# Optimization experiments

Measured on AMD Instinct MI355X. Metric: run time of the kernel, lower is better.

## Reference

```python
import jax, jax.numpy as jnp
import numpy as np
from jax import lax

K = 32768          # queue size
C = 100            # num_classes == len(cls_num_list1)
B = 1024           # batch size (features.shape[0] - K)
D = 128            # embedding dim
ALPHA = 0.05; BETA = 1.0; GAMMA = 1.0; SUPT = 1.0
T = 0.07; BASE_T = 0.07   # base_temperature defaults to temperature
SMOOTH = 0.0; EPS = 1e-12


def setup_inputs() -> dict:
    key = jax.random.key(0)
    k1, k2, k3, k4 = jax.random.split(key, 4)
    features = jax.random.normal(k1, (B + K, D), dtype=jnp.float32)
    features = features / jnp.linalg.norm(features, axis=1, keepdims=True)  # contrastive feats are L2-normalized
    centers = jax.random.normal(k2, (C, D), dtype=jnp.float32)
    centers = centers / jnp.linalg.norm(centers, axis=1, keepdims=True)
    sup_logits = jax.random.normal(k3, (B, C), dtype=jnp.float32)
    labels = jax.random.randint(k4, (B + K,), 0, C, dtype=jnp.int32)
    return {"features": features, "sup_logits": sup_logits, "centers": centers, "labels": labels}


def _loss(features, sup_logits, centers, labels):
    f32 = features.dtype
    lab_c = jnp.arange(C, dtype=labels.dtype)
    lab1 = jnp.concatenate([labels[:B], lab_c])                 # [B+C]
    mask = (labels[:B, None] == labels[None, :]).astype(f32)    # [B, B+K]
    mask1 = (lab1[:B, None] == lab1[None, :]).astype(f32)       # [B, B+C]
    # class counts over batch+queue (batch_cls_count) and batch+centers (batch_cls_count1)
    cls_count = jnp.zeros((C,), f32).at[labels].add(1.0)
    cls_count1 = jnp.zeros((C,), f32).at[lab1].add(1.0)
    diag = jnp.arange(B)
    logits_mask = jnp.ones((B, B + K), f32).at[diag, diag].set(0.0)
    logits_mask1 = jnp.ones((B, B + C), f32).at[diag, diag].set(0.0)
    mask = mask * logits_mask
    mask1 = mask1 * logits_mask1

    # ---- branch 1: batch anchors vs [batch, class centers] ----
    feats1 = jnp.concatenate([features[:B], centers], axis=0)   # [B+C, D]
    logits1 = (features[:B] @ feats1.T) / T                     # [B, B+C]
    logits1 = logits1 - lax.stop_gradient(logits1.max(axis=1, keepdims=True))
    exp1 = jnp.exp(logits1) * logits_mask1
    w1 = cls_count1[lab1][None, :] - mask1                      # per-instance class weight
    denom1 = (exp1 / w1).sum(axis=1, keepdims=True)
    log_prob1 = logits1 - jnp.log(denom1 + EPS)
    loss1 = -jnp.mean((mask1 * log_prob1).sum(1) / mask1.sum(1))

    # ---- branch 2: [sup_logits, batch anchors vs batch+queue] ----
    adc = (features[:B] @ features.T) / T                       # [B, B+K]
    logits = jnp.concatenate([sup_logits / SUPT, adc], axis=1)  # [B, C+B+K] (self.weight is None)
    logits = logits - lax.stop_gradient(logits.max(axis=1, keepdims=True))
    one_hot = jax.nn.one_hot(labels[:B], C, dtype=f32)
    one_hot = SMOOTH / (C - 1) * (1.0 - one_hot) + (1.0 - SMOOTH) * one_hot
    mask_full = jnp.concatenate([one_hot * BETA, mask * ALPHA], axis=1)
    lmask_full = jnp.concatenate([jnp.ones((B, C), f32), GAMMA * logits_mask], axis=1)
    expl = jnp.exp(logits) * lmask_full
    lab_full = jnp.concatenate([lab_c, labels])                 # [C+B+K]
    w = cls_count[lab_full][None, :] - mask_full
    denom = (expl / w).sum(axis=1, keepdims=True)
    log_prob = logits - jnp.log(denom + EPS)
    loss2 = -(T / BASE_T) * jnp.mean((mask_full * log_prob).sum(1) / mask_full.sum(1))
    return loss1 + loss2


def reference(features, sup_logits, centers, labels):
    return _loss(features, sup_logits, centers, labels)
```

## Files before the change

kernel.cpp:

```cpp
#include <hip/hip_runtime.h>
#include <math.h>

#define KQ   32768
#define CC   100
#define BB   1024
#define DD   128
#define NTOT (BB + KQ)
#define CB_CENT 1056
#define NCB  1060
#define NHIST 33
#define NCG2 132
#define CG_SUP 141
#define NSL  141

#define INV_T  14.285714285714286f
#define K2E    20.609929f
#define ALPHA  0.05f
#define EPSV   1e-12f

typedef __attribute__((ext_vector_type(8)))  short          short8;
typedef __attribute__((ext_vector_type(8)))  unsigned short ushort8;
typedef __attribute__((ext_vector_type(16))) float          float16;

__device__ __forceinline__ unsigned short f2bf_rne(float f) {
    unsigned int u = __float_as_uint(f);
    return (unsigned short)((u + 0x7FFFu + ((u >> 16) & 1u)) >> 16);
}


__global__ __launch_bounds__(256) void prep_k(const float* __restrict__ feats,
                                              const float* __restrict__ centers,
                                              const int* __restrict__ labels,
                                              unsigned short* __restrict__ X2,
                                              int* __restrict__ cntP,
                                              int* __restrict__ cntB) {
    const int b = blockIdx.x, t = threadIdx.x;
    if (b >= NCB) {
        const int h = b - NCB;
        __shared__ int hA[CC], hB[CC];
        if (t < CC) { hA[t] = 0; hB[t] = 0; }
        __syncthreads();
        const int base = h * 1024;
#pragma unroll
        for (int q = 0; q < 4; ++q) {
            int l = labels[base + q * 256 + t];
            atomicAdd(&hA[l], 1);
            if (h == 0) atomicAdd(&hB[l], 1);
        }
        __syncthreads();
        if (t < 128) {
            cntP[h * 128 + t] = (t < CC) ? hA[t] : 0;
            if (h == 0) cntB[t] = (t < CC) ? hB[t] : 0;
        }
        return;
    }
    __shared__ unsigned short sm[8 * 66 * 8];
    const int rl = t >> 3, c8 = t & 7;
    const int r = b * 32 + rl;
    const float* src;
    if (r < NTOT)            src = &feats[(size_t)r * DD];
    else if (r < NTOT + CC)  src = &centers[(size_t)(r - NTOT) * DD];
    else                     src = nullptr;
#pragma unroll
    for (int s = 0; s < 2; ++s) {
        const int c8p = c8 + 8 * s;
        float v[8];
        if (src) {
            const float4* p = (const float4*)(src + c8p * 8);
            float4 q0 = p[0], q1 = p[1];
            v[0]=q0.x; v[1]=q0.y; v[2]=q0.z; v[3]=q0.w;
            v[4]=q1.x; v[5]=q1.y; v[6]=q1.z; v[7]=q1.w;
        } else {
#pragma unroll
            for (int j = 0; j < 8; ++j) v[j] = 0.f;
        }
        ushort8 H;
#pragma unroll
        for (int m = 0; m < 8; ++m) H[m] = f2bf_rne(v[m]);
        const int ks = c8p >> 1, lh = c8p & 1;
        *(ushort8*)&sm[(ks * 66 + rl + 32 * lh) * 8] = H;
    }
    __syncthreads();
    ushort8* dst = (ushort8*)((char*)X2 + (size_t)b * 8192);
#pragma unroll
    for (int j = 0; j < 2; ++j) {
        const int idx = j * 256 + t;
        const int ks = idx >> 6, ln = idx & 63;
        dst[idx] = *(const ushort8*)&sm[(ks * 66 + ln) * 8];
    }
}

__device__ __forceinline__ void epi_tile(
    const float16& acc, int cb, int lc, float rn, float drm, bool checkDiag,
    int half, int ln, int growbase, const int* rlab, float* sS, float* sN)
{
    const int ccol = cb * 32 + ln;
#pragma unroll
    for (int reg = 0; reg < 16; ++reg) {
        int ro = (reg & 3) + 8 * (reg >> 2) + 4 * half;
        float a  = acc[reg];
        float mf = (lc == rlab[reg]) ? 1.f : 0.f;
        float wgt = fmaf(mf, drm, rn);
        if (checkDiag) {
            bool d = (ccol == growbase + ro);
            wgt = d ? 0.f : wgt;
            mf  = d ? 0.f : mf;
        }
        float e = exp2f(fmaf(a, K2E, -K2E));
        sS[reg] = fmaf(e, wgt, sS[reg]);
        sN[reg] = fmaf(mf, a, sN[reg]);
    }
}

__device__ __forceinline__ void pair_tiles(
    const char* Xb, int cb0, int cb1,
    int lc0, float rn0, float drm0, bool dg0,
    int lc1, float rn1, float drm1, bool dg1,
    int lane, int half, int ln, int growbase,
    const short8* Ah, const int* rlab, float* sS, float* sN)
{
    const size_t b0 = (size_t)cb0 * 8192 + (size_t)lane * 16;
    const size_t b1 = (size_t)cb1 * 8192 + (size_t)lane * 16;
    float16 a0, a1;
#pragma unroll
    for (int reg = 0; reg < 16; ++reg) { a0[reg] = 0.f; a1[reg] = 0.f; }
#pragma unroll
    for (int ks = 0; ks < 8; ++ks) {
        short8 B0 = *(const short8*)(Xb + b0 + (size_t)ks * 1024);
        short8 B1 = *(const short8*)(Xb + b1 + (size_t)ks * 1024);
        a0 = __builtin_amdgcn_mfma_f32_32x32x16_bf16(Ah[ks], B0, a0, 0, 0, 0);
        a1 = __builtin_amdgcn_mfma_f32_32x32x16_bf16(Ah[ks], B1, a1, 0, 0, 0);
    }
    epi_tile(a0, cb0, lc0, rn0, drm0, dg0, half, ln, growbase, rlab, sS, sN);
    epi_tile(a1, cb1, lc1, rn1, drm1, dg1, half, ln, growbase, rlab, sS, sN);
}

__global__ __launch_bounds__(256) void gemm_k(
    const unsigned short* __restrict__ X2, const int* __restrict__ labels,
    const int* __restrict__ cntP, const int* __restrict__ cntB,
    const float* __restrict__ sup,
    float* __restrict__ pS, float* __restrict__ pN,
    float* __restrict__ supS, float* __restrict__ supLi) {
    const int b = blockIdx.x;
    const int xcd = b & 7, l = b >> 3;
    const int rt = l & 7, ci = l >> 3;
    const int cg = xcd + 8 * ci;
    if (cg > CG_SUP) return;

    const int tid = threadIdx.x;
    const int lane = tid & 63, w = tid >> 6;
    const int half = lane >> 5, ln = lane & 31;
    const char* Xb = (const char*)X2;

    __shared__ float cntAF[128], rnA[128], drmA[128], rn1S[128], drm1S[128];
    if (tid < 128) {
        int s = 0;
#pragma unroll
        for (int h = 0; h < NHIST; ++h) s += cntP[h * 128 + tid];
        float cf = (float)s;
        cntAF[tid] = cf;
        float rn = __builtin_amdgcn_rcpf(fmaxf(cf, 1.f));
        rnA[tid] = (s > 0) ? __builtin_amdgcn_rcpf(cf) : 0.f;
        drmA[tid] = (s > 0) ? (__builtin_amdgcn_rcpf(cf - ALPHA) - rnA[tid]) : 0.f;
        (void)rn;
        int sb = cntB[tid];
        float c1 = (float)(sb + 1);
        float rn1 = __builtin_amdgcn_rcpf(c1);
        rn1S[tid] = rn1;
        drm1S[tid] = __builtin_amdgcn_rcpf(fmaxf(c1 - 1.f, 1.f)) - rn1;
    }
    __syncthreads();

    if (cg == CG_SUP) {
        const int g = rt * 4 + w;
        const int c0 = lane, c1 = lane + 64;
        float n0 = cntAF[c0];
        float rA0 = __builtin_amdgcn_rcpf(n0);
        float rAm0 = __builtin_amdgcn_rcpf(fmaxf(n0 - 1.f, 1.f));
        float rA1 = 0.f, rAm1 = 0.f;
        if (lane < 36) {
            float n1 = cntAF[c1];
            rA1 = __builtin_amdgcn_rcpf(n1);
            rAm1 = __builtin_amdgcn_rcpf(fmaxf(n1 - 1.f, 1.f));
        }
        for (int rr = 0; rr < 32; ++rr) {
            int row = g * 32 + rr;
            int li = labels[row];
            const float* srow = &sup[(size_t)row * CC];
            float v0 = srow[c0];
            float s = __expf(v0 - INV_T) * ((c0 == li) ? rAm0 : rA0);
            float liv = (c0 == li) ? v0 : 0.f;
            if (lane < 36) {
                float v1 = srow[c1];
                s += __expf(v1 - INV_T) * ((c1 == li) ? rAm1 : rA1);
                liv += (c1 == li) ? v1 : 0.f;
            }
#pragma unroll
            for (int off = 1; off < 64; off <<= 1) {
                s += __shfl_xor(s, off, 64);
                liv += __shfl_xor(liv, off, 64);
            }
            if (lane == 0) { supS[row] = s; supLi[row] = liv; }
        }
        return;
    }

    const int rb = rt * 4 + w;
    const int growbase = rt * 128 + w * 32;
    short8 Ah[8];
    {
        size_t abase = (size_t)rb * 8192 + (size_t)lane * 16;
#pragma unroll
        for (int ks = 0; ks < 8; ++ks)
            Ah[ks] = *(const short8*)(Xb + abase + (size_t)ks * 1024);
    }
    int rlab[16];
#pragma unroll
    for (int reg = 0; reg < 16; ++reg) {
        int ro = (reg & 3) + 8 * (reg >> 2) + 4 * half;
        rlab[reg] = labels[growbase + ro];
    }
    float sS[16], sN[16];
#pragma unroll
    for (int reg = 0; reg < 16; ++reg) { sS[reg] = 0.f; sN[reg] = 0.f; }

    const bool isB2 = (cg < NCG2);
    const int t1 = cg - NCG2;
    if (isB2) {
#pragma unroll
        for (int p = 0; p < 4; ++p) {
            const int cb0 = cg * 8 + 2 * p, cb1 = cb0 + 1;
            int lc0 = labels[cb0 * 32 + ln];
            int lc1 = labels[cb1 * 32 + ln];
            float rn0 = rnA[lc0], drm0 = drmA[lc0];
            float rn1 = rnA[lc1], drm1 = drmA[lc1];
            pair_tiles(Xb, cb0, cb1, lc0, rn0, drm0, cb0 == rb,
                       lc1, rn1, drm1, cb1 == rb,
                       lane, half, ln, growbase, Ah, rlab, sS, sN);
        }
    } else {
        const bool isBatch = (t1 < 8);
#pragma unroll
        for (int p = 0; p < 2; ++p) {
            int cb0, cb1, lc0, lc1;
            if (isBatch) {
                cb0 = t1 * 4 + 2 * p; cb1 = cb0 + 1;
                lc0 = labels[cb0 * 32 + ln];
                lc1 = labels[cb1 * 32 + ln];
            } else {
                cb0 = CB_CENT + 2 * p; cb1 = cb0 + 1;
                int q0 = cb0 * 32 + ln - NTOT, q1 = cb1 * 32 + ln - NTOT;
                lc0 = (q0 < CC) ? q0 : -1;
                lc1 = (q1 < CC) ? q1 : -1;
            }
            float rn0 = (lc0 >= 0) ? rn1S[lc0] : 0.f;
            float drm0 = (lc0 >= 0) ? drm1S[lc0] : 0.f;
            float rn1 = (lc1 >= 0) ? rn1S[lc1] : 0.f;
            float drm1 = (lc1 >= 0) ? drm1S[lc1] : 0.f;
            pair_tiles(Xb, cb0, cb1, lc0, rn0, drm0, isBatch && (cb0 == rb),
                       lc1, rn1, drm1, isBatch && (cb1 == rb),
                       lane, half, ln, growbase, Ah, rlab, sS, sN);
        }
    }
    const int slice = isB2 ? cg : (NCG2 + t1);
#pragma unroll
    for (int reg = 0; reg < 16; ++reg) {
        float a = sS[reg], c = sN[reg];
#pragma unroll
        for (int off = 1; off < 32; off <<= 1) {
            a += __shfl_xor(a, off, 64);
            c += __shfl_xor(c, off, 64);
        }
        if (ln == 0) {
            int ro = (reg & 3) + 8 * (reg >> 2) + 4 * half;
            int grow = growbase + ro;
            pS[(size_t)slice * BB + grow] = a;
            pN[(size_t)slice * BB + grow] = c;
        }
    }
}

__global__ __launch_bounds__(1024) void finalize_k(
    const int* __restrict__ labels,
    const int* __restrict__ cntP, const int* __restrict__ cntB,
    const float* __restrict__ pS, const float* __restrict__ pN,
    const float* __restrict__ supS, const float* __restrict__ supLi,
    float* __restrict__ out) {
    const int t = threadIdx.x;
    __shared__ float cntA[128];
    if (t < 128) {
        int s = 0;
#pragma unroll
        for (int h = 0; h < NHIST; ++h) s += cntP[h * 128 + t];
        cntA[t] = (float)s;
    }
    __syncthreads();
    const int li = labels[t];
    float S2 = supS[t], N2 = 0.f;
#pragma unroll 4
    for (int c = 0; c < NCG2; ++c) {
        S2 += pS[(size_t)c * BB + t];
        N2 += pN[(size_t)c * BB + t];
    }
    float S1 = 0.f, N1v = 0.f;
#pragma unroll
    for (int c = NCG2; c < NSL; ++c) {
        S1 += pS[(size_t)c * BB + t];
        N1v += pN[(size_t)c * BB + t];
    }
    N2 *= INV_T; N1v *= INV_T;
    float sli = supLi[t];
    float cA = cntA[li];
    float msum2 = fmaf(ALPHA, cA - 1.f, 1.f);
    float loss2 = -(fmaf(ALPHA, N2, sli) / msum2 - INV_T - logf(S2 + EPSV));
    float loss1 = -(N1v / (float)cntB[li] - INV_T - logf(S1 + EPSV));
    float s = loss1 + loss2;
    __shared__ float buf[16];
#pragma unroll
    for (int off = 1; off < 64; off <<= 1) s += __shfl_xor(s, off, 64);
    if ((t & 63) == 0) buf[t >> 6] = s;
    __syncthreads();
    if (t < 64) {
        float x = (t < 16) ? buf[t] : 0.f;
#pragma unroll
        for (int off = 1; off < 16; off <<= 1) x += __shfl_xor(x, off, 64);
        if (t == 0) out[0] = x / (float)BB;
    }
}

extern "C" void kernel_launch(void* const* d_in, const int* in_sizes, int n_in,
                              void* d_out, int out_size, void* d_ws, size_t ws_size,
                              hipStream_t stream) {
    const float* feats   = (const float*)d_in[0];
    const float* sup     = (const float*)d_in[1];
    const float* centers = (const float*)d_in[2];
    const int*   labels  = (const int*)d_in[3];
    float* out = (float*)d_out;
    char*  wsb = (char*)d_ws;

    const size_t X2_BYTES = (size_t)NCB * 8192;
    unsigned short* X2 = (unsigned short*)wsb;
    char* base2 = wsb + X2_BYTES;
    int* cntP = (int*)base2;
    int* cntB = cntP + NHIST * 128;
    float* pS = (float*)(cntB + 128);
    float* pN = pS + (size_t)NSL * BB;
    float* supS  = pN + (size_t)NSL * BB;
    float* supLi = supS + BB;

    prep_k<<<NCB + NHIST, 256, 0, stream>>>(feats, centers, labels, X2, cntP, cntB);
    gemm_k<<<8 * 8 * 18, 256, 0, stream>>>(X2, labels, cntP, cntB, sup,
                                           pS, pN, supS, supLi);
    finalize_k<<<1, 1024, 0, stream>>>(labels, cntP, cntB, pS, pN, supS, supLi, out);
}
```

Measured before the change: 136.7 us.

## Fuse finalize into gemm kernel via last-block atomic ticket

Drops the separate single-block finalize launch. Each active gemm block increments a global ticket after writing its partial sums, and the last block to arrive does the final row reduction and loss sum using 256 threads over 4 rows each. The ticket is reset in prep_k. The sup-logits path also batches four rows of loads before the exp and shuffle reductions so more loads are in flight. This saves one kernel launch gap but adds an atomic and a fence to every block, and the tail reduction now runs on 256 threads instead of 1024.

```diff
diff --git a/kernel.cpp b/kernel.cpp
--- a/kernel.cpp
+++ b/kernel.cpp
@@ -12,6 +12,7 @@
 #define NCG2 132
 #define CG_SUP 141
 #define NSL  141
+#define NACT 1136
 
 #define INV_T  14.285714285714286f
 #define K2E    20.609929f
@@ -33,7 +34,8 @@
                                               const int* __restrict__ labels,
                                               unsigned short* __restrict__ X2,
                                               int* __restrict__ cntP,
-                                              int* __restrict__ cntB) {
+                                              int* __restrict__ cntB,
+                                              unsigned int* __restrict__ ticket) {
     const int b = blockIdx.x, t = threadIdx.x;
     if (b >= NCB) {
         const int h = b - NCB;
@@ -52,6 +54,7 @@
             cntP[h * 128 + t] = (t < CC) ? hA[t] : 0;
             if (h == 0) cntB[t] = (t < CC) ? hB[t] : 0;
         }
+        if (h == 0 && t == 128) *ticket = 0u;
         return;
     }
     __shared__ unsigned short sm[8 * 66 * 8];
@@ -140,7 +143,8 @@
     const int* __restrict__ cntP, const int* __restrict__ cntB,
     const float* __restrict__ sup,
     float* __restrict__ pS, float* __restrict__ pN,
-    float* __restrict__ supS, float* __restrict__ supLi) {
+    float* __restrict__ supS, float* __restrict__ supLi,
+    unsigned int* __restrict__ ticket, float* __restrict__ out) {
     const int b = blockIdx.x;
     const int xcd = b & 7, l = b >> 3;
     const int rt = l & 7, ci = l >> 3;
@@ -159,10 +163,8 @@
         for (int h = 0; h < NHIST; ++h) s += cntP[h * 128 + tid];
         float cf = (float)s;
         cntAF[tid] = cf;
-        float rn = __builtin_amdgcn_rcpf(fmaxf(cf, 1.f));
         rnA[tid] = (s > 0) ? __builtin_amdgcn_rcpf(cf) : 0.f;
         drmA[tid] = (s > 0) ? (__builtin_amdgcn_rcpf(cf - ALPHA) - rnA[tid]) : 0.f;
-        (void)rn;
         int sb = cntB[tid];
         float c1 = (float)(sb + 1);
         float rn1 = __builtin_amdgcn_rcpf(c1);
@@ -183,149 +185,152 @@
             rA1 = __builtin_amdgcn_rcpf(n1);
             rAm1 = __builtin_amdgcn_rcpf(fmaxf(n1 - 1.f, 1.f));
         }
-        for (int rr = 0; rr < 32; ++rr) {
-            int row = g * 32 + rr;
-            int li = labels[row];
-            const float* srow = &sup[(size_t)row * CC];
-            float v0 = srow[c0];
-            float s = __expf(v0 - INV_T) * ((c0 == li) ? rAm0 : rA0);
-            float liv = (c0 == li) ? v0 : 0.f;
-            if (lane < 36) {
-                float v1 = srow[c1];
-                s += __expf(v1 - INV_T) * ((c1 == li) ? rAm1 : rA1);
-                liv += (c1 == li) ? v1 : 0.f;
-            }
-#pragma unroll
-            for (int off = 1; off < 64; off <<= 1) {
-                s += __shfl_xor(s, off, 64);
-                liv += __shfl_xor(liv, off, 64);
-            }
-            if (lane == 0) { supS[row] = s; supLi[row] = liv; }
-        }
-        return;
-    }
-
-    const int rb = rt * 4 + w;
-    const int growbase = rt * 128 + w * 32;
-    short8 Ah[8];
-    {
-        size_t abase = (size_t)rb * 8192 + (size_t)lane * 16;
-#pragma unroll
-        for (int ks = 0; ks < 8; ++ks)
-            Ah[ks] = *(const short8*)(Xb + abase + (size_t)ks * 1024);
-    }
-    int rlab[16];
-#pragma unroll
-    for (int reg = 0; reg < 16; ++reg) {
-        int ro = (reg & 3) + 8 * (reg >> 2) + 4 * half;
-        rlab[reg] = labels[growbase + ro];
-    }
-    float sS[16], sN[16];
-#pragma unroll
-    for (int reg = 0; reg < 16; ++reg) { sS[reg] = 0.f; sN[reg] = 0.f; }
-
-    const bool isB2 = (cg < NCG2);
-    const int t1 = cg - NCG2;
-    if (isB2) {
-#pragma unroll
-        for (int p = 0; p < 4; ++p) {
-            const int cb0 = cg * 8 + 2 * p, cb1 = cb0 + 1;
-            int lc0 = labels[cb0 * 32 + ln];
-            int lc1 = labels[cb1 * 32 + ln];
-            float rn0 = rnA[lc0], drm0 = drmA[lc0];
-            float rn1 = rnA[lc1], drm1 = drmA[lc1];
-            pair_tiles(Xb, cb0, cb1, lc0, rn0, drm0, cb0 == rb,
-                       lc1, rn1, drm1, cb1 == rb,
-                       lane, half, ln, growbase, Ah, rlab, sS, sN);
+        for (int rq = 0; rq < 8; ++rq) {
+            float v0[4], v1[4];
+            int li[4];
+#pragma unroll
+            for (int k = 0; k < 4; ++k) {
+                int row = g * 32 + rq * 4 + k;
+                li[k] = labels[row];
+                const float* srow = &sup[(size_t)row * CC];
+                v0[k] = srow[c0];
+                v1[k] = (lane < 36) ? srow[c1] : 0.f;
+            }
+#pragma unroll
+            for (int k = 0; k < 4; ++k) {
+                int row = g * 32 + rq * 4 + k;
+                float s = __expf(v0[k] - INV_T) * ((c0 == li[k]) ? rAm0 : rA0);
+                float liv = (c0 == li[k]) ? v0[k] : 0.f;
+                if (lane < 36) {
+                    s += __expf(v1[k] - INV_T) * ((c1 == li[k]) ? rAm1 : rA1);
+                    liv += (c1 == li[k]) ? v1[k] : 0.f;
+                }
+#pragma unroll
+                for (int off = 1; off < 64; off <<= 1) {
+                    s += __shfl_xor(s, off, 64);
+                    liv += __shfl_xor(liv, off, 64);
+                }
+                if (lane == 0) { supS[row] = s; supLi[row] = liv; }
+            }
         }
     } else {
-        const bool isBatch = (t1 < 8);
-#pragma unroll
-        for (int p = 0; p < 2; ++p) {
-            int cb0, cb1, lc0, lc1;
-            if (isBatch) {
-                cb0 = t1 * 4 + 2 * p; cb1 = cb0 + 1;
-                lc0 = labels[cb0 * 32 + ln];
-                lc1 = labels[cb1 * 32 + ln];
-            } else {
-                cb0 = CB_CENT + 2 * p; cb1 = cb0 + 1;
-                int q0 = cb0 * 32 + ln - NTOT, q1 = cb1 * 32 + ln - NTOT;
-                lc0 = (q0 < CC) ? q0 : -1;
-                lc1 = (q1 < CC) ? q1 : -1;
-            }
-            float rn0 = (lc0 >= 0) ? rn1S[lc0] : 0.f;
-            float drm0 = (lc0 >= 0) ? drm1S[lc0] : 0.f;
-            float rn1 = (lc1 >= 0) ? rn1S[lc1] : 0.f;
-            float drm1 = (lc1 >= 0) ? drm1S[lc1] : 0.f;
-            pair_tiles(Xb, cb0, cb1, lc0, rn0, drm0, isBatch && (cb0 == rb),
-                       lc1, rn1, drm1, isBatch && (cb1 == rb),
-                       lane, half, ln, growbase, Ah, rlab, sS, sN);
-        }
-    }
-    const int slice = isB2 ? cg : (NCG2 + t1);
-#pragma unroll
-    for (int reg = 0; reg < 16; ++reg) {
-        float a = sS[reg], c = sN[reg];
-#pragma unroll
-        for (int off = 1; off < 32; off <<= 1) {
-            a += __shfl_xor(a, off, 64);
-            c += __shfl_xor(c, off, 64);
-        }
-        if (ln == 0) {
+        const int rb = rt * 4 + w;
+        const int growbase = rt * 128 + w * 32;
+        short8 Ah[8];
+        {
+            size_t abase = (size_t)rb * 8192 + (size_t)lane * 16;
+#pragma unroll
+            for (int ks = 0; ks < 8; ++ks)
+                Ah[ks] = *(const short8*)(Xb + abase + (size_t)ks * 1024);
+        }
+        int rlab[16];
+#pragma unroll
+        for (int reg = 0; reg < 16; ++reg) {
             int ro = (reg & 3) + 8 * (reg >> 2) + 4 * half;
-            int grow = growbase + ro;
-            pS[(size_t)slice * BB + grow] = a;
-            pN[(size_t)slice * BB + grow] = c;
-        }
-    }
-}
-
-__global__ __launch_bounds__(1024) void finalize_k(
-    const int* __restrict__ labels,
-    const int* __restrict__ cntP, const int* __restrict__ cntB,
-    const float* __restrict__ pS, const float* __restrict__ pN,
-    const float* __restrict__ supS, const float* __restrict__ supLi,
-    float* __restrict__ out) {
-    const int t = threadIdx.x;
-    __shared__ float cntA[128];
-    if (t < 128) {
-        int s = 0;
-#pragma unroll
-        for (int h = 0; h < NHIST; ++h) s += cntP[h * 128 + t];
-        cntA[t] = (float)s;
-    }
-    __syncthreads();
-    const int li = labels[t];
-    float S2 = supS[t], N2 = 0.f;
+            rlab[reg] = labels[growbase + ro];
+        }
+        float sS[16], sN[16];
+#pragma unroll
+        for (int reg = 0; reg < 16; ++reg) { sS[reg] = 0.f; sN[reg] = 0.f; }
+
+        const bool isB2 = (cg < NCG2);
+        const int t1 = cg - NCG2;
+        if (isB2) {
+#pragma unroll
+            for (int p = 0; p < 4; ++p) {
+                const int cb0 = cg * 8 + 2 * p, cb1 = cb0 + 1;
+                int lc0 = labels[cb0 * 32 + ln];
+                int lc1 = labels[cb1 * 32 + ln];
+                pair_tiles(Xb, cb0, cb1, lc0, rnA[lc0], drmA[lc0], cb0 == rb,
+                           lc1, rnA[lc1], drmA[lc1], cb1 == rb,
+                           lane, half, ln, growbase, Ah, rlab, sS, sN);
+            }
+        } else {
+            const bool isBatch = (t1 < 8);
+#pragma unroll
+            for (int p = 0; p < 2; ++p) {
+                int cb0, cb1, lc0, lc1;
+                if (isBatch) {
+                    cb0 = t1 * 4 + 2 * p; cb1 = cb0 + 1;
+                    lc0 = labels[cb0 * 32 + ln];
+                    lc1 = labels[cb1 * 32 + ln];
+                } else {
+                    cb0 = CB_CENT + 2 * p; cb1 = cb0 + 1;
+                    int q0 = cb0 * 32 + ln - NTOT, q1 = cb1 * 32 + ln - NTOT;
+                    lc0 = (q0 < CC) ? q0 : -1;
+                    lc1 = (q1 < CC) ? q1 : -1;
+                }
+                float rn0 = (lc0 >= 0) ? rn1S[lc0] : 0.f;
+                float drm0 = (lc0 >= 0) ? drm1S[lc0] : 0.f;
+                float rn1 = (lc1 >= 0) ? rn1S[lc1] : 0.f;
+                float drm1 = (lc1 >= 0) ? drm1S[lc1] : 0.f;
+                pair_tiles(Xb, cb0, cb1, lc0, rn0, drm0, isBatch && (cb0 == rb),
+                           lc1, rn1, drm1, isBatch && (cb1 == rb),
+                           lane, half, ln, growbase, Ah, rlab, sS, sN);
+            }
+        }
+        const int slice = isB2 ? cg : (NCG2 + t1);
+#pragma unroll
+        for (int reg = 0; reg < 16; ++reg) {
+            float a = sS[reg], c = sN[reg];
+#pragma unroll
+            for (int off = 1; off < 32; off <<= 1) {
+                a += __shfl_xor(a, off, 64);
+                c += __shfl_xor(c, off, 64);
+            }
+            if (ln == 0) {
+                int ro = (reg & 3) + 8 * (reg >> 2) + 4 * half;
+                int grow = growbase + ro;
+                pS[(size_t)slice * BB + grow] = a;
+                pN[(size_t)slice * BB + grow] = c;
+            }
+        }
+    }
+
+    __syncthreads();
+    __threadfence();
+    __shared__ unsigned int lastFlag;
+    if (tid == 0) {
+        unsigned int old = __hip_atomic_fetch_add(ticket, 1u, __ATOMIC_ACQ_REL,
+                                                  __HIP_MEMORY_SCOPE_AGENT);
+        lastFlag = (old == NACT - 1) ? 1u : 0u;
+    }
+    __syncthreads();
+    if (!lastFlag) return;
+    __threadfence();
+
+    float lsum = 0.f;
+#pragma unroll
+    for (int q = 0; q < 4; ++q) {
+        const int row = q * 256 + tid;
+        const int li = labels[row];
+        float S2 = supS[row], N2 = 0.f;
 #pragma unroll 4
-    for (int c = 0; c < NCG2; ++c) {
-        S2 += pS[(size_t)c * BB + t];
-        N2 += pN[(size_t)c * BB + t];
-    }
-    float S1 = 0.f, N1v = 0.f;
-#pragma unroll
-    for (int c = NCG2; c < NSL; ++c) {
-        S1 += pS[(size_t)c * BB + t];
-        N1v += pN[(size_t)c * BB + t];
-    }
-    N2 *= INV_T; N1v *= INV_T;
-    float sli = supLi[t];
-    float cA = cntA[li];
-    float msum2 = fmaf(ALPHA, cA - 1.f, 1.f);
-    float loss2 = -(fmaf(ALPHA, N2, sli) / msum2 - INV_T - logf(S2 + EPSV));
-    float loss1 = -(N1v / (float)cntB[li] - INV_T - logf(S1 + EPSV));
-    float s = loss1 + loss2;
-    __shared__ float buf[16];
-#pragma unroll
-    for (int off = 1; off < 64; off <<= 1) s += __shfl_xor(s, off, 64);
-    if ((t & 63) == 0) buf[t >> 6] = s;
-    __syncthreads();
-    if (t < 64) {
-        float x = (t < 16) ? buf[t] : 0.f;
-#pragma unroll
-        for (int off = 1; off < 16; off <<= 1) x += __shfl_xor(x, off, 64);
-        if (t == 0) out[0] = x / (float)BB;
-    }
+        for (int c = 0; c < NCG2; ++c) {
+            S2 += pS[(size_t)c * BB + row];
+            N2 += pN[(size_t)c * BB + row];
+        }
+        float S1 = 0.f, N1v = 0.f;
+#pragma unroll
+        for (int c = NCG2; c < NSL; ++c) {
+            S1 += pS[(size_t)c * BB + row];
+            N1v += pN[(size_t)c * BB + row];
+        }
+        N2 *= INV_T; N1v *= INV_T;
+        float sli = supLi[row];
+        float cA = cntAF[li];
+        float msum2 = fmaf(ALPHA, cA - 1.f, 1.f);
+        float loss2 = -(fmaf(ALPHA, N2, sli) / msum2 - INV_T - logf(S2 + EPSV));
+        float cb1 = cntAF[li] - 0.f;  (void)cb1;
+        float loss1 = -(N1v / (float)cntB[li] - INV_T - logf(S1 + EPSV));
+        lsum += loss1 + loss2;
+    }
+    __shared__ float rbuf[4];
+#pragma unroll
+    for (int off = 1; off < 64; off <<= 1) lsum += __shfl_xor(lsum, off, 64);
+    if (lane == 0) rbuf[w] = lsum;
+    __syncthreads();
+    if (tid == 0) out[0] = (rbuf[0] + rbuf[1] + rbuf[2] + rbuf[3]) / (float)BB;
 }
 
 extern "C" void kernel_launch(void* const* d_in, const int* in_sizes, int n_in,
@@ -343,13 +348,13 @@
     char* base2 = wsb + X2_BYTES;
     int* cntP = (int*)base2;
     int* cntB = cntP + NHIST * 128;
-    float* pS = (float*)(cntB + 128);
+    unsigned int* ticket = (unsigned int*)(cntB + 128);
+    float* pS = (float*)(ticket + 128);
     float* pN = pS + (size_t)NSL * BB;
     float* supS  = pN + (size_t)NSL * BB;
     float* supLi = supS + BB;
 
-    prep_k<<<NCB + NHIST, 256, 0, stream>>>(feats, centers, labels, X2, cntP, cntB);
+    prep_k<<<NCB + NHIST, 256, 0, stream>>>(feats, centers, labels, X2, cntP, cntB, ticket);
     gemm_k<<<8 * 8 * 18, 256, 0, stream>>>(X2, labels, cntP, cntB, sup,
-                                           pS, pN, supS, supLi);
-    finalize_k<<<1, 1024, 0, stream>>>(labels, cntP, cntB, pS, pN, supS, supLi, out);
-}
+                                           pS, pN, supS, supLi, ticket, out);
+}
```

Result: slower. 267.1 us (+95.4%).
